# Kernel optimization log

Measured on AMD Instinct MI355X. Metric: run time of the kernel, lower is better.

The kernel has to match this reference:

```python
import jax, jax.numpy as jnp
import numpy as np

D_MODEL = 768
MIMO_RANK = 4


def setup_inputs() -> dict:
    key = jax.random.key(0)
    ks = jax.random.split(key, 6)
    B, T, D, R = 2, 2048, D_MODEL, MIMO_RANK
    x = jax.random.normal(ks[0], (B, T, D), dtype=jnp.float32)
    norm_w = jnp.ones((D,), dtype=jnp.float32)
    W_in = jax.random.normal(ks[1], (D * R * 2, D), dtype=jnp.float32) * 0.02
    W_out = jax.random.normal(ks[2], (D, D), dtype=jnp.float32) * 0.02
    a_param = jax.random.normal(ks[3], (D, R, 2), dtype=jnp.float32) * 0.12
    b_param = jax.random.normal(ks[4], (D, R, 2), dtype=jnp.float32) * 0.15
    c_param = jax.random.normal(ks[5], (D, R, 2), dtype=jnp.float32) * 0.15
    return {"x": x, "norm_w": norm_w, "W_in": W_in, "W_out": W_out,
            "a_param": a_param, "b_param": b_param, "c_param": c_param}


def reference(x, norm_w, W_in, W_out, a_param, b_param, c_param):
    B, T, D = x.shape
    R = a_param.shape[1]
    # RMSNorm
    xn = x * jax.lax.rsqrt(jnp.mean(x * x, axis=-1, keepdims=True) + 1e-6) * norm_w
    # in_proj -> interleaved complex MIMO input u: [B,T,D,R,2]
    u = (xn @ W_in.T).reshape(B, T, D, R, 2)
    # coefficients (tanh-bounded; |a| scaled by 0.97 for stability)
    a = jnp.tanh(a_param) * 0.97
    b = jnp.tanh(b_param)
    c = jnp.tanh(c_param)
    ac = jax.lax.complex(a[..., 0], a[..., 1])  # [D,R]
    bc = jax.lax.complex(b[..., 0], b[..., 1])
    cc = jax.lax.complex(c[..., 0], c[..., 1])
    uc = jax.lax.complex(u[..., 0], u[..., 1])  # [B,T,D,R]
    # linear complex recurrence s_t = a * s_{t-1} + b * u_t, zero init state,
    # parallelized with an associative scan over time.
    bu = bc[None, None] * uc
    A = jnp.broadcast_to(ac[None, None], bu.shape)

    def comb(l, r):
        return (l[0] * r[0], r[0] * l[1] + r[1])

    _, s = jax.lax.associative_scan(comb, (A, bu), axis=1)  # [B,T,D,R] complex
    # output mix: real part of c * h, summed over MIMO rank -> [B,T,D]
    y = jnp.real(cc[None, None] * s).sum(axis=-1)
    return y @ W_out.T
```

## Files before the change

kernel.cpp:

```cpp
#include <hip/hip_runtime.h>
#include <hip/hip_bf16.h>
#include <stdint.h>

#define BATCH 2
#define TT 2048
#define DM 768
#define RR 4
#define M_TOK 4096
#define NFEAT 6144
#define NCH 6144
#define CHUNK 64
#define NCHUNK 32

typedef __attribute__((ext_vector_type(8))) short short8;
typedef __attribute__((ext_vector_type(4))) float float4v;

__device__ inline float bf2f(uint32_t bits16) {
    union { uint32_t u; float f; } x; x.u = bits16 << 16; return x.f;
}

typedef const __attribute__((address_space(1))) void* gptr_t;
typedef __attribute__((address_space(3))) void* lptr_t;

__device__ inline void async_ld16(const void* g, void* l) {
    __builtin_amdgcn_global_load_lds((gptr_t)(uintptr_t)g, (lptr_t)(uintptr_t)l,
                                     16, 0, 0);
}

__device__ inline uint2 pack4bf(float a, float b, float c, float d) {
    union { __hip_bfloat16 h[4]; uint2 u; } o;
    o.h[0] = __float2bfloat16(a); o.h[1] = __float2bfloat16(b);
    o.h[2] = __float2bfloat16(c); o.h[3] = __float2bfloat16(d);
    return o.u;
}

__device__ inline float2 cmul(float2 a, float2 b) {
    return make_float2(a.x * b.x - a.y * b.y, a.x * b.y + a.y * b.x);
}
__device__ inline float2 cmad(float2 a, float2 b, float2 c) {
    return make_float2(a.x * b.x - a.y * b.y + c.x,
                       a.x * b.y + a.y * b.x + c.y);
}
__device__ inline float2 csq(float2 a) {
    return make_float2(a.x * a.x - a.y * a.y, 2.f * a.x * a.y);
}

__device__ inline void cstep(float& sr, float& si, float2 a, float2 bb,
                             uint32_t uw) {
    float ur = bf2f(uw & 0xffffu), ui = bf2f(uw >> 16);
    float tr = bb.x * ur - bb.y * ui;
    float ti = bb.x * ui + bb.y * ur;
    float nr = a.x * sr - a.y * si + tr;
    float ni = a.x * si + a.y * sr + ti;
    sr = nr; si = ni;
}

__global__ __launch_bounds__(256) void prep_rms(
    const float* __restrict__ x, const float* __restrict__ w,
    const float* __restrict__ W_in, const float* __restrict__ W_out,
    const float* __restrict__ ap, const float* __restrict__ bp,
    const float* __restrict__ cp,
    __hip_bfloat16* __restrict__ xn,
    __hip_bfloat16* __restrict__ Win_bf, __hip_bfloat16* __restrict__ Wout_bf,
    float2* __restrict__ ac, float2* __restrict__ bc,
    float2* __restrict__ cc, float2* __restrict__ aL) {
    int bid = blockIdx.x;
    int tid = threadIdx.x;
    if (bid < M_TOK) {
        __shared__ float wsum[3];
        float4 v = make_float4(0.f, 0.f, 0.f, 0.f);
        if (tid < 192) v = ((const float4*)(x + (size_t)bid * DM))[tid];
        float ss = v.x * v.x + v.y * v.y + v.z * v.z + v.w * v.w;
        #pragma unroll
        for (int o = 1; o < 64; o <<= 1) ss += __shfl_xor(ss, o);
        if (tid < 192 && (tid & 63) == 0) wsum[tid >> 6] = ss;
        __syncthreads();
        if (tid < 192) {
            float tot = wsum[0] + wsum[1] + wsum[2];
            float scale = rsqrtf(tot * (1.f / DM) + 1e-6f);
            float4 wv = ((const float4*)w)[tid];
            ((uint2*)(xn + (size_t)bid * DM))[tid] =
                pack4bf(v.x * scale * wv.x, v.y * scale * wv.y,
                        v.z * scale * wv.z, v.w * scale * wv.w);
        }
        return;
    }
    const int N1 = NFEAT * DM / 4;
    const int N2 = DM * DM / 4;
    int i = (bid - M_TOK) * 256 + tid;
    if (i < N1) {
        float4 v = ((const float4*)W_in)[i];
        ((uint2*)Win_bf)[i] = pack4bf(v.x, v.y, v.z, v.w);
    } else if (i < N1 + N2) {
        int k = i - N1;
        float4 v = ((const float4*)W_out)[k];
        ((uint2*)Wout_bf)[k] = pack4bf(v.x, v.y, v.z, v.w);
    }
    if (i < DM * RR) {
        float ar = tanhf(ap[2 * i])     * 0.97f;
        float ai = tanhf(ap[2 * i + 1]) * 0.97f;
        ac[i] = make_float2(ar, ai);
        bc[i] = make_float2(tanhf(bp[2 * i]), tanhf(bp[2 * i + 1]));
        cc[i] = make_float2(tanhf(cp[2 * i]), tanhf(cp[2 * i + 1]));
        float xr = ar, xi = ai;
        #pragma unroll
        for (int k = 0; k < 6; ++k) {
            float nr = xr * xr - xi * xi;
            float ni = 2.f * xr * xi;
            xr = nr; xi = ni;
        }
        aL[i] = make_float2(xr, xi);
    }
}

__global__ __launch_bounds__(512, 4) void gemm_in(
    const __hip_bfloat16* __restrict__ A, const __hip_bfloat16* __restrict__ B,
    __hip_bfloat16* __restrict__ C, int K) {
    constexpr int BM = 128, BN = 128, BK = 64;
    constexpr int CPR = BK / 8;
    constexpr int ldc = NFEAT;
    __shared__ __attribute__((aligned(16))) __hip_bfloat16
        lds2[2][BM * BK + BN * BK];
    const int tid  = threadIdx.x;
    const int lane = tid & 63;
    const int wave = tid >> 6;
    const int quad = lane >> 4;
    const int l15  = lane & 15;
    const int wm = (wave >> 2) * 64;
    const int wn = (wave & 3) * 32;
    const int m0 = blockIdx.y * BM;
    const int n0 = blockIdx.x * BN;

    float4v acc[4][2] = {};

    auto stage = [&](int bi, int t) {
        __hip_bfloat16* sA = lds2[bi];
        __hip_bfloat16* sB = lds2[bi] + BM * BK;
        const int k0 = t * BK;
        #pragma unroll
        for (int it = 0; it < BM * CPR / 512; ++it) {
            int p = it * 512 + tid;
            int row = p >> 3;
            int cg = (p & 7) ^ (row & 7);
            async_ld16(A + (size_t)(m0 + row) * K + k0 + cg * 8, sA + p * 8);
        }
        #pragma unroll
        for (int it = 0; it < BN * CPR / 512; ++it) {
            int p = it * 512 + tid;
            int row = p >> 3;
            int cg = (p & 7) ^ (row & 7);
            async_ld16(B + (size_t)(n0 + row) * K + k0 + cg * 8, sB + p * 8);
        }
    };

    const int nt = K / BK;
    stage(0, 0);
    for (int t = 0; t < nt; ++t) {
        const int cur = t & 1;
        if (t + 1 < nt) {
            stage(cur ^ 1, t + 1);
            asm volatile("s_waitcnt vmcnt(4)" ::: "memory");
        } else {
            asm volatile("s_waitcnt vmcnt(0)" ::: "memory");
        }
        asm volatile("s_barrier" ::: "memory");
        const __hip_bfloat16* lA = lds2[cur];
        const __hip_bfloat16* lB = lds2[cur] + BM * BK;
        #pragma unroll
        for (int s = 0; s < BK / 32; ++s) {
            short8 af[4], bfr[2];
            #pragma unroll
            for (int i = 0; i < 4; ++i) {
                int r = wm + i * 16 + l15;
                int c = (s * 4 + quad) ^ (r & 7);
                af[i] = *(const short8*)(lA + r * BK + c * 8);
            }
            #pragma unroll
            for (int j = 0; j < 2; ++j) {
                int r = wn + j * 16 + l15;
                int c = (s * 4 + quad) ^ (r & 7);
                bfr[j] = *(const short8*)(lB + r * BK + c * 8);
            }
            #pragma unroll
            for (int i = 0; i < 4; ++i)
                #pragma unroll
                for (int j = 0; j < 2; ++j)
                    acc[i][j] = __builtin_amdgcn_mfma_f32_16x16x32_bf16(
                        af[i], bfr[j], acc[i][j], 0, 0, 0);
        }
        asm volatile("s_waitcnt lgkmcnt(0)" ::: "memory");
        asm volatile("s_barrier" ::: "memory");
    }
    #pragma unroll
    for (int i = 0; i < 4; ++i)
        #pragma unroll
        for (int j = 0; j < 2; ++j)
            #pragma unroll
            for (int rg = 0; rg < 4; ++rg) {
                int row = m0 + wm + i * 16 + quad * 4 + rg;
                int col = n0 + wn + j * 16 + l15;
                C[(size_t)row * ldc + col] = __float2bfloat16(acc[i][j][rg]);
            }
}

__global__ __launch_bounds__(256, 4) void gemm_out(
    const __hip_bfloat16* __restrict__ A, const __hip_bfloat16* __restrict__ B,
    float* __restrict__ C, int K) {
    constexpr int BM = 64, BN = 64, BK = 64;
    constexpr int CPR = BK / 8;
    constexpr int ldc = DM;
    __shared__ __attribute__((aligned(16))) __hip_bfloat16
        lds2[2][(BM + BN) * BK];
    const int tid  = threadIdx.x;
    const int lane = tid & 63;
    const int wave = tid >> 6;
    const int quad = lane >> 4;
    const int l15  = lane & 15;
    const int wm = (wave >> 1) * 32;
    const int wn = (wave & 1) * 32;
    const int m0 = blockIdx.y * BM;
    const int n0 = blockIdx.x * BN;

    float4v acc[2][2] = {};

    auto stage = [&](int bi, int t) {
        __hip_bfloat16* sA = lds2[bi];
        __hip_bfloat16* sB = lds2[bi] + BM * BK;
        const int k0 = t * BK;
        #pragma unroll
        for (int it = 0; it < BM * CPR / 256; ++it) {
            int p = it * 256 + tid;
            int row = p >> 3;
            int cg = (p & 7) ^ (row & 7);
            async_ld16(A + (size_t)(m0 + row) * K + k0 + cg * 8, sA + p * 8);
        }
        #pragma unroll
        for (int it = 0; it < BN * CPR / 256; ++it) {
            int p = it * 256 + tid;
            int row = p >> 3;
            int cg = (p & 7) ^ (row & 7);
            async_ld16(B + (size_t)(n0 + row) * K + k0 + cg * 8, sB + p * 8);
        }
    };

    const int nt = K / BK;
    stage(0, 0);
    for (int t = 0; t < nt; ++t) {
        const int cur = t & 1;
        if (t + 1 < nt) {
            stage(cur ^ 1, t + 1);
            asm volatile("s_waitcnt vmcnt(4)" ::: "memory");
        } else {
            asm volatile("s_waitcnt vmcnt(0)" ::: "memory");
        }
        asm volatile("s_barrier" ::: "memory");
        const __hip_bfloat16* lA = lds2[cur];
        const __hip_bfloat16* lB = lds2[cur] + BM * BK;
        #pragma unroll
        for (int s = 0; s < BK / 32; ++s) {
            short8 af[2], bfr[2];
            #pragma unroll
            for (int i = 0; i < 2; ++i) {
                int r = wm + i * 16 + l15;
                int c = (s * 4 + quad) ^ (r & 7);
                af[i] = *(const short8*)(lA + r * BK + c * 8);
            }
            #pragma unroll
            for (int j = 0; j < 2; ++j) {
                int r = wn + j * 16 + l15;
                int c = (s * 4 + quad) ^ (r & 7);
                bfr[j] = *(const short8*)(lB + r * BK + c * 8);
            }
            #pragma unroll
            for (int i = 0; i < 2; ++i)
                #pragma unroll
                for (int j = 0; j < 2; ++j)
                    acc[i][j] = __builtin_amdgcn_mfma_f32_16x16x32_bf16(
                        af[i], bfr[j], acc[i][j], 0, 0, 0);
        }
        asm volatile("s_waitcnt lgkmcnt(0)" ::: "memory");
        asm volatile("s_barrier" ::: "memory");
    }
    #pragma unroll
    for (int i = 0; i < 2; ++i)
        #pragma unroll
        for (int j = 0; j < 2; ++j)
            #pragma unroll
            for (int rg = 0; rg < 4; ++rg) {
                int row = m0 + wm + i * 16 + quad * 4 + rg;
                int col = n0 + wn + j * 16 + l15;
                C[(size_t)row * ldc + col] = acc[i][j][rg];
            }
}

__global__ __launch_bounds__(256) void scan_local2(
    const uint4* __restrict__ u4,
    const float2* __restrict__ ac, const float2* __restrict__ bc,
    const float2* __restrict__ cc,
    __hip_bfloat16* __restrict__ y_local,
    float2* __restrict__ chunkEnd) {
    __shared__ float2 se[1024];
    const int tid   = threadIdx.x;
    const int d_loc = tid & 31;
    const int s8    = tid >> 5;
    const int bd    = blockIdx.x;
    const int b     = bd >= 24;
    const int dg    = bd - b * 24;
    const int d_g   = dg * 32 + d_loc;
    const int cb    = d_g * RR;
    const int j     = blockIdx.y;

    float2 a0 = ac[cb], a1 = ac[cb + 1], a2 = ac[cb + 2], a3 = ac[cb + 3];
    float2 b0 = bc[cb], b1 = bc[cb + 1], b2 = bc[cb + 2], b3 = bc[cb + 3];
    float2 c0 = cc[cb], c1 = cc[cb + 1], c2 = cc[cb + 2], c3 = cc[cb + 3];

    const int token0 = b * TT + j * CHUNK + s8 * 8;
    const size_t base = (size_t)token0 * DM + d_g;

    uint4 uw[8];
    #pragma unroll
    for (int i = 0; i < 8; ++i) uw[i] = u4[base + (size_t)i * DM];
    float s0r = 0, s0i = 0, s1r = 0, s1i = 0;
    float s2r = 0, s2i = 0, s3r = 0, s3i = 0;
    float yloc[8];
    #pragma unroll
    for (int i = 0; i < 8; ++i) {
        cstep(s0r, s0i, a0, b0, uw[i].x);
        cstep(s1r, s1i, a1, b1, uw[i].y);
        cstep(s2r, s2i, a2, b2, uw[i].z);
        cstep(s3r, s3i, a3, b3, uw[i].w);
        yloc[i] = c0.x * s0r - c0.y * s0i + c1.x * s1r - c1.y * s1i
                + c2.x * s2r - c2.y * s2i + c3.x * s3r - c3.y * s3i;
    }
    se[tid * 4]     = make_float2(s0r, s0i);
    se[tid * 4 + 1] = make_float2(s1r, s1i);
    se[tid * 4 + 2] = make_float2(s2r, s2i);
    se[tid * 4 + 3] = make_float2(s3r, s3i);
    __syncthreads();

    float2 aE0 = csq(csq(csq(a0))), aE1 = csq(csq(csq(a1)));
    float2 aE2 = csq(csq(csq(a2))), aE3 = csq(csq(csq(a3)));
    float2 C0 = make_float2(0, 0), C1 = C0, C2 = C0, C3 = C0;
    for (int k = 0; k < s8; ++k) {
        int kb = (k * 32 + d_loc) * 4;
        C0 = cmad(C0, aE0, se[kb]);
        C1 = cmad(C1, aE1, se[kb + 1]);
        C2 = cmad(C2, aE2, se[kb + 2]);
        C3 = cmad(C3, aE3, se[kb + 3]);
    }
    if (s8 == 7) {
        size_t eb = (size_t)j * NCH + b * (DM * RR) + cb;
        chunkEnd[eb]     = cmad(C0, aE0, make_float2(s0r, s0i));
        chunkEnd[eb + 1] = cmad(C1, aE1, make_float2(s1r, s1i));
        chunkEnd[eb + 2] = cmad(C2, aE2, make_float2(s2r, s2i));
        chunkEnd[eb + 3] = cmad(C3, aE3, make_float2(s3r, s3i));
    }
    float2 q0 = cmul(cmul(c0, C0), a0);
    float2 q1 = cmul(cmul(c1, C1), a1);
    float2 q2 = cmul(cmul(c2, C2), a2);
    float2 q3 = cmul(cmul(c3, C3), a3);
    #pragma unroll
    for (int i = 0; i < 8; ++i) {
        float yv = yloc[i] + q0.x + q1.x + q2.x + q3.x;
        y_local[base + (size_t)i * DM] = __float2bfloat16(yv);
        q0 = cmul(q0, a0); q1 = cmul(q1, a1);
        q2 = cmul(q2, a2); q3 = cmul(q3, a3);
    }
}

__global__ __launch_bounds__(256) void carry_scan(
    float2* __restrict__ chunkEnd,
    const float2* __restrict__ aLp) {
    int ch = blockIdx.x * 256 + threadIdx.x;
    int dr = (ch >= DM * RR) ? ch - DM * RR : ch;
    float2 aL = aLp[dr];
    float2 K = make_float2(0.f, 0.f);
    for (int j = 0; j < NCHUNK; ++j) {
        size_t idx = (size_t)j * NCH + ch;
        float2 e = chunkEnd[idx];
        chunkEnd[idx] = K;
        K = cmad(K, aL, e);
    }
}

__global__ __launch_bounds__(256) void scan_fix(
    __hip_bfloat16* __restrict__ y_local,
    const float2* __restrict__ ac, const float2* __restrict__ cc,
    const float2* __restrict__ carry) {
    const int tid   = threadIdx.x;
    const int d_loc = tid & 31;
    const int s8    = tid >> 5;
    const int bd    = blockIdx.x;
    const int b     = bd >= 24;
    const int dg    = bd - b * 24;
    const int d_g   = dg * 32 + d_loc;
    const int cb    = d_g * RR;
    const int j     = blockIdx.y;
    const size_t kb = (size_t)j * NCH + b * (DM * RR) + cb;

    float2 a0 = ac[cb], a1 = ac[cb + 1], a2 = ac[cb + 2], a3 = ac[cb + 3];
    float2 c0 = cc[cb], c1 = cc[cb + 1], c2 = cc[cb + 2], c3 = cc[cb + 3];
    float2 K0 = carry[kb],     K1 = carry[kb + 1];
    float2 K2 = carry[kb + 2], K3 = carry[kb + 3];

    float2 aE0 = csq(csq(csq(a0))), aE1 = csq(csq(csq(a1)));
    float2 aE2 = csq(csq(csq(a2))), aE3 = csq(csq(csq(a3)));
    float2 q0 = cmul(cmul(c0, K0), a0);
    float2 q1 = cmul(cmul(c1, K1), a1);
    float2 q2 = cmul(cmul(c2, K2), a2);
    float2 q3 = cmul(cmul(c3, K3), a3);
    for (int t = 0; t < s8; ++t) {
        q0 = cmul(q0, aE0); q1 = cmul(q1, aE1);
        q2 = cmul(q2, aE2); q3 = cmul(q3, aE3);
    }
    const int token0 = b * TT + j * CHUNK + s8 * 8;
    const size_t base = (size_t)token0 * DM + d_g;
    #pragma unroll
    for (int i = 0; i < 8; ++i) {
        size_t idx = base + (size_t)i * DM;
        float yv = bf2f(((const uint16_t*)y_local)[idx])
                 + q0.x + q1.x + q2.x + q3.x;
        y_local[idx] = __float2bfloat16(yv);
        q0 = cmul(q0, a0); q1 = cmul(q1, a1);
        q2 = cmul(q2, a2); q3 = cmul(q3, a3);
    }
}

extern "C" void kernel_launch(void* const* d_in, const int* in_sizes, int n_in,
                              void* d_out, int out_size, void* d_ws,
                              size_t ws_size, hipStream_t stream) {
    const float* x      = (const float*)d_in[0];
    const float* norm_w = (const float*)d_in[1];
    const float* W_in   = (const float*)d_in[2];
    const float* W_out  = (const float*)d_in[3];
    const float* a_p    = (const float*)d_in[4];
    const float* b_p    = (const float*)d_in[5];
    const float* c_p    = (const float*)d_in[6];
    float* out = (float*)d_out;

    char* ws = (char*)d_ws;
    size_t off = 0;
    auto alloc = [&](size_t bytes) {
        void* p = ws + off;
        off += (bytes + 255) & ~(size_t)255;
        return p;
    };
    __hip_bfloat16* Win_bf  = (__hip_bfloat16*)alloc((size_t)NFEAT * DM * 2);
    __hip_bfloat16* Wout_bf = (__hip_bfloat16*)alloc((size_t)DM * DM * 2);
    __hip_bfloat16* xn      = (__hip_bfloat16*)alloc((size_t)M_TOK * DM * 2);
    __hip_bfloat16* u       = (__hip_bfloat16*)alloc((size_t)M_TOK * NFEAT * 2);
    __hip_bfloat16* y_local = (__hip_bfloat16*)alloc((size_t)M_TOK * DM * 2);
    float2* ac = (float2*)alloc((size_t)DM * RR * 8);
    float2* bc = (float2*)alloc((size_t)DM * RR * 8);
    float2* cc = (float2*)alloc((size_t)DM * RR * 8);
    float2* aL = (float2*)alloc((size_t)DM * RR * 8);
    float2* chunkEnd = (float2*)alloc((size_t)NCHUNK * NCH * 8);

    {
        int cast_blocks = ((NFEAT * DM + DM * DM) / 4 + 255) / 256;
        prep_rms<<<M_TOK + cast_blocks, 256, 0, stream>>>(
            x, norm_w, W_in, W_out, a_p, b_p, c_p,
            xn, Win_bf, Wout_bf, ac, bc, cc, aL);
    }
    gemm_in<<<dim3(NFEAT / 128, M_TOK / 128), 512, 0, stream>>>(
        xn, Win_bf, u, DM);
    scan_local2<<<dim3(48, NCHUNK), 256, 0, stream>>>(
        (const uint4*)u, ac, bc, cc, y_local, chunkEnd);
    carry_scan<<<NCH / 256, 256, 0, stream>>>(chunkEnd, aL);
    scan_fix<<<dim3(48, NCHUNK), 256, 0, stream>>>(
        y_local, ac, cc, chunkEnd);
    gemm_out<<<dim3(DM / 64, M_TOK / 64), 256, 0, stream>>>(
        y_local, Wout_bf, out, DM);
}
```

Before: 169.0 us.

## Fuse chunk-local scan into input GEMM epilogue, drop u buffer

The input projection GEMM now stages its bf16 output tile in LDS with a swizzled layout and runs the chunk-local complex scan directly in the epilogue. Each 128x128 tile covers 16 channels and two 64-token chunks, so it writes y_local and chunk-end states itself. This removes the 48MB u intermediate, its global write and reread, and one kernel launch. In exchange the GEMM epilogue gets longer, with extra syncs and register pressure that may reduce occupancy.

```diff
diff --git a/kernel.cpp b/kernel.cpp
--- a/kernel.cpp
+++ b/kernel.cpp
@@ -31,6 +31,12 @@
     union { __hip_bfloat16 h[4]; uint2 u; } o;
     o.h[0] = __float2bfloat16(a); o.h[1] = __float2bfloat16(b);
     o.h[2] = __float2bfloat16(c); o.h[3] = __float2bfloat16(d);
+    return o.u;
+}
+
+__device__ inline uint32_t pack2bf(float a, float b) {
+    union { __hip_bfloat16 h[2]; uint32_t u; } o;
+    o.h[0] = __float2bfloat16(a); o.h[1] = __float2bfloat16(b);
     return o.u;
 }
 
@@ -113,12 +119,16 @@
     }
 }
 
-__global__ __launch_bounds__(512, 4) void gemm_in(
-    const __hip_bfloat16* __restrict__ A, const __hip_bfloat16* __restrict__ B,
-    __hip_bfloat16* __restrict__ C, int K) {
+__global__ __launch_bounds__(512, 4) void gemm_in_scan(
+    const __hip_bfloat16* __restrict__ A,
+    const __hip_bfloat16* __restrict__ B,
+    const float2* __restrict__ ac, const float2* __restrict__ bc,
+    const float2* __restrict__ cc,
+    __hip_bfloat16* __restrict__ y_local,
+    float2* __restrict__ chunkEnd,
+    int K) {
     constexpr int BM = 128, BN = 128, BK = 64;
     constexpr int CPR = BK / 8;
-    constexpr int ldc = NFEAT;
     __shared__ __attribute__((aligned(16))) __hip_bfloat16
         lds2[2][BM * BK + BN * BK];
     const int tid  = threadIdx.x;
@@ -191,16 +201,98 @@
         asm volatile("s_waitcnt lgkmcnt(0)" ::: "memory");
         asm volatile("s_barrier" ::: "memory");
     }
+
+    uint32_t* up = (uint32_t*)lds2[0];
     #pragma unroll
     for (int i = 0; i < 4; ++i)
         #pragma unroll
-        for (int j = 0; j < 2; ++j)
-            #pragma unroll
-            for (int rg = 0; rg < 4; ++rg) {
-                int row = m0 + wm + i * 16 + quad * 4 + rg;
-                int col = n0 + wn + j * 16 + l15;
-                C[(size_t)row * ldc + col] = __float2bfloat16(acc[i][j][rg]);
-            }
+        for (int j = 0; j < 2; ++j) {
+            float s0 = __shfl_xor(acc[i][j][0], 1);
+            float s1 = __shfl_xor(acc[i][j][1], 1);
+            float s2 = __shfl_xor(acc[i][j][2], 1);
+            float s3 = __shfl_xor(acc[i][j][3], 1);
+            const bool odd = l15 & 1;
+            float lo0 = odd ? s2 : acc[i][j][0];
+            float hi0 = odd ? acc[i][j][2] : s0;
+            float lo1 = odd ? s3 : acc[i][j][1];
+            float hi1 = odd ? acc[i][j][3] : s1;
+            int row0 = wm + i * 16 + quad * 4 + (odd ? 2 : 0);
+            int row1 = row0 + 1;
+            int pr = (wn + j * 16 + (l15 & ~1)) >> 1;
+            int sl = pr & 3;
+            up[row0 * 64 + (((pr >> 2) ^ (row0 & 15)) << 2) + sl] =
+                pack2bf(lo0, hi0);
+            up[row1 * 64 + (((pr >> 2) ^ (row1 & 15)) << 2) + sl] =
+                pack2bf(lo1, hi1);
+        }
+    __syncthreads();
+
+    {
+        const int d_loc = tid & 15;
+        const int half  = (tid >> 4) & 1;
+        const int slice = tid >> 5;
+        const int d_g   = (n0 >> 3) + d_loc;
+        const int cb    = d_g * RR;
+        float2 a0 = ac[cb], a1 = ac[cb + 1], a2 = ac[cb + 2], a3 = ac[cb + 3];
+        float2 b0 = bc[cb], b1 = bc[cb + 1], b2 = bc[cb + 2], b3 = bc[cb + 3];
+        float2 c0 = cc[cb], c1 = cc[cb + 1], c2 = cc[cb + 2], c3 = cc[cb + 3];
+        const uint4* up4 = (const uint4*)lds2[0];
+        float2* se = (float2*)lds2[1];
+        const int rbase = half * 64 + slice * 4;
+
+        float s0r = 0, s0i = 0, s1r = 0, s1i = 0;
+        float s2r = 0, s2i = 0, s3r = 0, s3i = 0;
+        float yloc[4];
+        #pragma unroll
+        for (int i = 0; i < 4; ++i) {
+            int row = rbase + i;
+            uint4 uw = up4[row * 16 + (d_loc ^ (row & 15))];
+            cstep(s0r, s0i, a0, b0, uw.x);
+            cstep(s1r, s1i, a1, b1, uw.y);
+            cstep(s2r, s2i, a2, b2, uw.z);
+            cstep(s3r, s3i, a3, b3, uw.w);
+            yloc[i] = c0.x * s0r - c0.y * s0i + c1.x * s1r - c1.y * s1i
+                    + c2.x * s2r - c2.y * s2i + c3.x * s3r - c3.y * s3i;
+        }
+        const int sbase = ((half * 16 + slice) * 16 + d_loc) * 4;
+        se[sbase]     = make_float2(s0r, s0i);
+        se[sbase + 1] = make_float2(s1r, s1i);
+        se[sbase + 2] = make_float2(s2r, s2i);
+        se[sbase + 3] = make_float2(s3r, s3i);
+        __syncthreads();
+
+        float2 aE0 = csq(csq(a0)), aE1 = csq(csq(a1));
+        float2 aE2 = csq(csq(a2)), aE3 = csq(csq(a3));
+        float2 C0 = make_float2(0, 0), C1 = C0, C2 = C0, C3 = C0;
+        for (int k = 0; k < slice; ++k) {
+            int kb = ((half * 16 + k) * 16 + d_loc) * 4;
+            C0 = cmad(C0, aE0, se[kb]);
+            C1 = cmad(C1, aE1, se[kb + 1]);
+            C2 = cmad(C2, aE2, se[kb + 2]);
+            C3 = cmad(C3, aE3, se[kb + 3]);
+        }
+        if (slice == 15) {
+            const int bb = m0 >> 11;
+            const int j  = ((m0 & (TT - 1)) >> 6) + half;
+            size_t eb = (size_t)j * NCH + bb * (DM * RR) + cb;
+            chunkEnd[eb]     = cmad(C0, aE0, make_float2(s0r, s0i));
+            chunkEnd[eb + 1] = cmad(C1, aE1, make_float2(s1r, s1i));
+            chunkEnd[eb + 2] = cmad(C2, aE2, make_float2(s2r, s2i));
+            chunkEnd[eb + 3] = cmad(C3, aE3, make_float2(s3r, s3i));
+        }
+        float2 q0 = cmul(cmul(c0, C0), a0);
+        float2 q1 = cmul(cmul(c1, C1), a1);
+        float2 q2 = cmul(cmul(c2, C2), a2);
+        float2 q3 = cmul(cmul(c3, C3), a3);
+        size_t ybase = (size_t)(m0 + rbase) * DM + d_g;
+        #pragma unroll
+        for (int i = 0; i < 4; ++i) {
+            float yv = yloc[i] + q0.x + q1.x + q2.x + q3.x;
+            y_local[ybase + (size_t)i * DM] = __float2bfloat16(yv);
+            q0 = cmul(q0, a0); q1 = cmul(q1, a1);
+            q2 = cmul(q2, a2); q3 = cmul(q3, a3);
+        }
+    }
 }
 
 __global__ __launch_bounds__(256, 4) void gemm_out(
@@ -293,81 +385,6 @@
             }
 }
 
-__global__ __launch_bounds__(256) void scan_local2(
-    const uint4* __restrict__ u4,
-    const float2* __restrict__ ac, const float2* __restrict__ bc,
-    const float2* __restrict__ cc,
-    __hip_bfloat16* __restrict__ y_local,
-    float2* __restrict__ chunkEnd) {
-    __shared__ float2 se[1024];
-    const int tid   = threadIdx.x;
-    const int d_loc = tid & 31;
-    const int s8    = tid >> 5;
-    const int bd    = blockIdx.x;
-    const int b     = bd >= 24;
-    const int dg    = bd - b * 24;
-    const int d_g   = dg * 32 + d_loc;
-    const int cb    = d_g * RR;
-    const int j     = blockIdx.y;
-
-    float2 a0 = ac[cb], a1 = ac[cb + 1], a2 = ac[cb + 2], a3 = ac[cb + 3];
-    float2 b0 = bc[cb], b1 = bc[cb + 1], b2 = bc[cb + 2], b3 = bc[cb + 3];
-    float2 c0 = cc[cb], c1 = cc[cb + 1], c2 = cc[cb + 2], c3 = cc[cb + 3];
-
-    const int token0 = b * TT + j * CHUNK + s8 * 8;
-    const size_t base = (size_t)token0 * DM + d_g;
-
-    uint4 uw[8];
-    #pragma unroll
-    for (int i = 0; i < 8; ++i) uw[i] = u4[base + (size_t)i * DM];
-    float s0r = 0, s0i = 0, s1r = 0, s1i = 0;
-    float s2r = 0, s2i = 0, s3r = 0, s3i = 0;
-    float yloc[8];
-    #pragma unroll
-    for (int i = 0; i < 8; ++i) {
-        cstep(s0r, s0i, a0, b0, uw[i].x);
-        cstep(s1r, s1i, a1, b1, uw[i].y);
-        cstep(s2r, s2i, a2, b2, uw[i].z);
-        cstep(s3r, s3i, a3, b3, uw[i].w);
-        yloc[i] = c0.x * s0r - c0.y * s0i + c1.x * s1r - c1.y * s1i
-                + c2.x * s2r - c2.y * s2i + c3.x * s3r - c3.y * s3i;
-    }
-    se[tid * 4]     = make_float2(s0r, s0i);
-    se[tid * 4 + 1] = make_float2(s1r, s1i);
-    se[tid * 4 + 2] = make_float2(s2r, s2i);
-    se[tid * 4 + 3] = make_float2(s3r, s3i);
-    __syncthreads();
-
-    float2 aE0 = csq(csq(csq(a0))), aE1 = csq(csq(csq(a1)));
-    float2 aE2 = csq(csq(csq(a2))), aE3 = csq(csq(csq(a3)));
-    float2 C0 = make_float2(0, 0), C1 = C0, C2 = C0, C3 = C0;
-    for (int k = 0; k < s8; ++k) {
-        int kb = (k * 32 + d_loc) * 4;
-        C0 = cmad(C0, aE0, se[kb]);
-        C1 = cmad(C1, aE1, se[kb + 1]);
-        C2 = cmad(C2, aE2, se[kb + 2]);
-        C3 = cmad(C3, aE3, se[kb + 3]);
-    }
-    if (s8 == 7) {
-        size_t eb = (size_t)j * NCH + b * (DM * RR) + cb;
-        chunkEnd[eb]     = cmad(C0, aE0, make_float2(s0r, s0i));
-        chunkEnd[eb + 1] = cmad(C1, aE1, make_float2(s1r, s1i));
-        chunkEnd[eb + 2] = cmad(C2, aE2, make_float2(s2r, s2i));
-        chunkEnd[eb + 3] = cmad(C3, aE3, make_float2(s3r, s3i));
-    }
-    float2 q0 = cmul(cmul(c0, C0), a0);
-    float2 q1 = cmul(cmul(c1, C1), a1);
-    float2 q2 = cmul(cmul(c2, C2), a2);
-    float2 q3 = cmul(cmul(c3, C3), a3);
-    #pragma unroll
-    for (int i = 0; i < 8; ++i) {
-        float yv = yloc[i] + q0.x + q1.x + q2.x + q3.x;
-        y_local[base + (size_t)i * DM] = __float2bfloat16(yv);
-        q0 = cmul(q0, a0); q1 = cmul(q1, a1);
-        q2 = cmul(q2, a2); q3 = cmul(q3, a3);
-    }
-}
-
 __global__ __launch_bounds__(256) void carry_scan(
     float2* __restrict__ chunkEnd,
     const float2* __restrict__ aLp) {
@@ -448,7 +465,6 @@
     __hip_bfloat16* Win_bf  = (__hip_bfloat16*)alloc((size_t)NFEAT * DM * 2);
     __hip_bfloat16* Wout_bf = (__hip_bfloat16*)alloc((size_t)DM * DM * 2);
     __hip_bfloat16* xn      = (__hip_bfloat16*)alloc((size_t)M_TOK * DM * 2);
-    __hip_bfloat16* u       = (__hip_bfloat16*)alloc((size_t)M_TOK * NFEAT * 2);
     __hip_bfloat16* y_local = (__hip_bfloat16*)alloc((size_t)M_TOK * DM * 2);
     float2* ac = (float2*)alloc((size_t)DM * RR * 8);
     float2* bc = (float2*)alloc((size_t)DM * RR * 8);
@@ -462,10 +478,8 @@
             x, norm_w, W_in, W_out, a_p, b_p, c_p,
             xn, Win_bf, Wout_bf, ac, bc, cc, aL);
     }
-    gemm_in<<<dim3(NFEAT / 128, M_TOK / 128), 512, 0, stream>>>(
-        xn, Win_bf, u, DM);
-    scan_local2<<<dim3(48, NCHUNK), 256, 0, stream>>>(
-        (const uint4*)u, ac, bc, cc, y_local, chunkEnd);
+    gemm_in_scan<<<dim3(NFEAT / 128, M_TOK / 128), 512, 0, stream>>>(
+        xn, Win_bf, ac, bc, cc, y_local, chunkEnd, DM);
     carry_scan<<<NCH / 256, 256, 0, stream>>>(chunkEnd, aL);
     scan_fix<<<dim3(48, NCHUNK), 256, 0, stream>>>(
         y_local, ac, cc, chunkEnd);
```

Result: slower. 174.3 us (+3.1%).
